# Optimization experiments

Measured on AMD Instinct MI355X. Metric: run time of the kernel, lower is better.

## Reference

```python
import jax, jax.numpy as jnp
import numpy as np

N_NODES = 51200
N_GRAPHS = 64
NODES_PER_GRAPH = 800
N_EDGES = 819200
DIM_IN = 128
DIM_HIDDEN = 64
HEADS = 3
DIM_OUT = 64


def leaky(x, slope):
    return jnp.where(x >= 0, x, slope * x)


def setup_inputs() -> dict:
    key = jax.random.key(0)
    ks = jax.random.split(key, 12)
    s = lambda fan_in: 1.0 / np.sqrt(fan_in)
    X = jax.random.normal(ks[0], (N_NODES, DIM_IN), dtype=jnp.float32)
    edge_indices = jax.random.randint(ks[1], (2, N_EDGES), 0, N_NODES, dtype=jnp.int32)
    ptr = (jnp.arange(N_GRAPHS + 1, dtype=jnp.int32) * NODES_PER_GRAPH)
    # linearSeq: Linear(dim_in, dim_hidden) + LeakyReLU
    W1 = jax.random.uniform(ks[2], (DIM_IN, DIM_HIDDEN), jnp.float32, -s(DIM_IN), s(DIM_IN))
    b1 = jax.random.uniform(ks[3], (DIM_HIDDEN,), jnp.float32, -s(DIM_IN), s(DIM_IN))
    # GATConv params: lin_src/lin_dst (no bias), att_src/att_dst, bias (concat=False -> out_channels)
    W_src = jax.random.uniform(ks[4], (DIM_HIDDEN, HEADS * DIM_HIDDEN), jnp.float32, -s(DIM_HIDDEN), s(DIM_HIDDEN))
    W_dst = jax.random.uniform(ks[5], (DIM_HIDDEN, HEADS * DIM_HIDDEN), jnp.float32, -s(DIM_HIDDEN), s(DIM_HIDDEN))
    att_src = jax.random.normal(ks[6], (HEADS, DIM_HIDDEN), dtype=jnp.float32) * 0.1
    att_dst = jax.random.normal(ks[7], (HEADS, DIM_HIDDEN), dtype=jnp.float32) * 0.1
    gat_bias = jnp.zeros((DIM_HIDDEN,), dtype=jnp.float32)
    # linear_final: Linear(2*dim_hidden, dim_out)
    Wf = jax.random.uniform(ks[8], (2 * DIM_HIDDEN, DIM_OUT), jnp.float32, -s(2 * DIM_HIDDEN), s(2 * DIM_HIDDEN))
    bf = jax.random.uniform(ks[9], (DIM_OUT,), jnp.float32, -s(2 * DIM_HIDDEN), s(2 * DIM_HIDDEN))
    return {"X": X, "W1": W1, "b1": b1, "W_src": W_src, "W_dst": W_dst,
            "att_src": att_src, "att_dst": att_dst, "gat_bias": gat_bias,
            "Wf": Wf, "bf": bf, "edge_indices": edge_indices, "ptr": ptr}


def reference(X, W1, b1, W_src, W_dst, att_src, att_dst, gat_bias, Wf, bf, edge_indices, ptr):
    N = X.shape[0]
    src, dst = edge_indices[0], edge_indices[1]  # message flows src -> dst
    # input projection
    h = leaky(X @ W1 + b1, 0.01)                                  # [N, DH]
    # GATConv (heads=3, concat=False, add_self_loops=False)
    x_src = (h @ W_src).reshape(N, HEADS, DIM_HIDDEN)             # [N, H, C]
    x_dst = (h @ W_dst).reshape(N, HEADS, DIM_HIDDEN)
    a_src = jnp.einsum('nhc,hc->nh', x_src, att_src)              # [N, H]
    a_dst = jnp.einsum('nhc,hc->nh', x_dst, att_dst)
    logits = leaky(a_src[src] + a_dst[dst], 0.2)                  # [E, H]
    # segment softmax over incoming edges of each target node
    m = jax.ops.segment_max(logits, dst, num_segments=N)          # [N, H]
    e = jnp.exp(logits - m[dst])
    denom = jax.ops.segment_sum(e, dst, num_segments=N)           # [N, H]
    attn = e / denom[dst]                                         # [E, H]
    msg = x_src[src] * attn[..., None]                            # [E, H, C]
    agg = jax.ops.segment_sum(msg, dst, num_segments=N)           # [N, H, C]
    out = agg.mean(axis=1) + gat_bias                             # concat=False -> head mean
    # final head
    cat = jnp.concatenate([h, out], axis=1)                       # [N, 2*DH]
    y = leaky(cat, 0.01) @ Wf + bf                                # [N, DO]
    # aggregate_using_ptr: mean-pool nodes per graph using CSR ptr
    node_graph = jnp.searchsorted(ptr, jnp.arange(N), side='right') - 1
    sums = jax.ops.segment_sum(y, node_graph, num_segments=ptr.shape[0] - 1)
    counts = (ptr[1:] - ptr[:-1]).astype(y.dtype)
    pooled = sums / counts[:, None]                               # [n_graphs, DO]
    return pooled, attn
```

## Files before the change

kernel.cpp:

```cpp
#include <hip/hip_runtime.h>
#include <hip/hip_bf16.h>

#define N_NODES   51200
#define N_GRAPHS  64
#define N_EDGES   819200
#define DIM_IN    128
#define DH        64
#define HEADS     3
#define DIM_OUT   64
#define CAP       96
#define NPART     8
#define PART_SZ   (N_NODES / NPART)
#define SC_BLOCKS (NPART * (N_EDGES / 2048))
#define K1_BLOCKS (N_NODES / 64)
#define P2_BLOCKS 80

typedef __hip_bfloat16 bf16;
typedef short bf16x8 __attribute__((ext_vector_type(8)));
typedef float f32x4  __attribute__((ext_vector_type(4)));

__device__ __forceinline__ float b2f(bf16 x) { return __bfloat162float(x); }
__device__ __forceinline__ bf16  f2b(float x) { return __float2bfloat16(x); }
__device__ __forceinline__ short f2bs(float x) { return (short)__bfloat16_as_ushort(f2b(x)); }
__device__ __forceinline__ float leaky(float x, float s) { return x >= 0.f ? x : s * x; }
__device__ __forceinline__ float ldin(const void* p, size_t i, int f32) {
    return f32 ? ((const float*)p)[i] : b2f(((const bf16*)p)[i]);
}
__device__ __forceinline__ bf16x8 ld8(const void* p, size_t i, int f32) {
    if (!f32) return *((const bf16x8*)((const short*)p + i));
    const float* f = (const float*)p + i;
    bf16x8 r;
    #pragma unroll
    for (int j = 0; j < 8; ++j) r[j] = f2bs(f[j]);
    return r;
}

__global__ __launch_bounds__(256) void detect_kernel(const unsigned short* __restrict__ Xu,
                                                     int* __restrict__ flag) {
    __shared__ int cnt;
    int tid = threadIdx.x;
    if (tid == 0) cnt = 0;
    __syncthreads();
    int local = 0;
    for (int i = tid * 2; i < 8192; i += 512) {
        unsigned e = (Xu[i] >> 7) & 0xFF;
        if (e >= 110 && e <= 135) local++;
    }
    atomicAdd(&cnt, local);
    __syncthreads();
    if (tid == 0) *flag = (cnt < 2048) ? 1 : 0;
}

__global__ __launch_bounds__(256) void prep1_kernel(const void* __restrict__ W1,
                                                    const void* __restrict__ Wsrc,
                                                    const void* __restrict__ Wdst,
                                                    const void* __restrict__ att_src,
                                                    const void* __restrict__ att_dst,
                                                    const int* __restrict__ flagp,
                                                    short* __restrict__ W1t,
                                                    short* __restrict__ Wat) {
    const int f32 = *flagp;
    int idx = blockIdx.x * 256 + threadIdx.x;
    if (idx < 8192) {
        int n = idx >> 7, k = idx & 127;
        W1t[idx] = f2bs(ldin(W1, (size_t)k * 64 + n, f32));
    } else if (idx < 9216) {
        int j = idx - 8192;
        int n = j >> 6, k = j & 63;
        float v = 0.f;
        if (n < 3) {
            for (int c = 0; c < 64; ++c)
                v += ldin(Wsrc, (size_t)k * 192 + n * 64 + c, f32) * ldin(att_src, n * 64 + c, f32);
        } else if (n < 6) {
            for (int c = 0; c < 64; ++c)
                v += ldin(Wdst, (size_t)k * 192 + (n - 3) * 64 + c, f32) * ldin(att_dst, (n - 3) * 64 + c, f32);
        }
        Wat[j] = f2bs(v);
    }
}

__global__ __launch_bounds__(256) void mega_kernel(const int* __restrict__ src,
                                                   const int* __restrict__ dst,
                                                   int* __restrict__ cursor,
                                                   unsigned short* __restrict__ bucket,
                                                   const void* __restrict__ X,
                                                   const short* __restrict__ W1t,
                                                   const short* __restrict__ Wat,
                                                   const void* __restrict__ b1,
                                                   const void* __restrict__ Wsrc,
                                                   const void* __restrict__ Wf,
                                                   const int* __restrict__ flagp,
                                                   bf16* __restrict__ h_bf,
                                                   unsigned char* __restrict__ h8,
                                                   float* __restrict__ a_src4,
                                                   float* __restrict__ a_dst4,
                                                   short* __restrict__ Wspt,
                                                   short* __restrict__ Wft) {
    if (blockIdx.x < SC_BLOCKS) {
        const int p = blockIdx.x & (NPART - 1);
        const int slice = blockIdx.x >> 3;
        const int lo = p * PART_SZ, hi = lo + PART_SZ;
        const int base = slice * 2048 + threadIdx.x;
        #pragma unroll
        for (int t = 0; t < 8; ++t) {
            int e = base + t * 256;
            int d = dst[e];
            if (d >= lo && d < hi) {
                int pos = atomicAdd(&cursor[d], 1);
                if (pos < CAP) bucket[(size_t)d * CAP + pos] = (unsigned short)src[e];
            }
        }
        return;
    }
    if (blockIdx.x >= SC_BLOCKS + K1_BLOCKS) {
        const int f32 = *flagp;
        int idx = (blockIdx.x - SC_BLOCKS - K1_BLOCKS) * 256 + threadIdx.x;
        if (idx < 12288) {
            int col = idx / 192;
            int rem = idx - col * 192;
            int hh = rem >> 6, kk = rem & 63;
            Wspt[idx] = f2bs(ldin(Wsrc, (size_t)kk * 192 + hh * 64 + col, f32) * (1.0f / 3.0f));
        } else {
            int j = idx - 12288;
            int n = j >> 7, k = j & 127;
            Wft[j] = f2bs(ldin(Wf, (size_t)k * 64 + n, f32));
        }
        return;
    }
    const int f32 = *flagp;
    __shared__ short hs[64 * 72];
    const int tid  = threadIdx.x;
    const int w    = tid >> 6;
    const int lane = tid & 63;
    const int lm   = lane & 15;
    const int q    = lane >> 4;
    const int row0 = (blockIdx.x - SC_BLOCKS) * 64;

    const float bias = ldin(b1, w * 16 + lm, f32);
    for (int mt = 0; mt < 4; ++mt) {
        f32x4 acc = {0.f, 0.f, 0.f, 0.f};
        #pragma unroll
        for (int kc = 0; kc < 4; ++kc) {
            bf16x8 a = ld8(X, (size_t)(row0 + mt * 16 + lm) * 128 + kc * 32 + q * 8, f32);
            bf16x8 b = *((const bf16x8*)(W1t + (size_t)(w * 16 + lm) * 128 + kc * 32 + q * 8));
            acc = __builtin_amdgcn_mfma_f32_16x16x32_bf16(a, b, acc, 0, 0, 0);
        }
        #pragma unroll
        for (int r = 0; r < 4; ++r) {
            int row = mt * 16 + q * 4 + r;
            float v = leaky(acc[r] + bias, 0.01f);
            short hv = f2bs(v);
            hs[row * 72 + w * 16 + lm] = hv;
            h_bf[(size_t)(row0 + row) * 64 + w * 16 + lm] = __ushort_as_bfloat16((unsigned short)hv);
            h8[(size_t)(row0 + row) * 64 + w * 16 + lm] =
                (unsigned char)__builtin_amdgcn_cvt_pk_fp8_f32(v, 0.f, 0, false);
        }
    }
    __syncthreads();

    {
        const int mt = w;
        bf16x8 a0  = *((const bf16x8*)(hs + (mt * 16 + lm) * 72 + q * 8));
        bf16x8 a1  = *((const bf16x8*)(hs + (mt * 16 + lm) * 72 + 32 + q * 8));
        bf16x8 b0  = *((const bf16x8*)(Wat + (size_t)lm * 64 + q * 8));
        bf16x8 b1v = *((const bf16x8*)(Wat + (size_t)lm * 64 + 32 + q * 8));
        f32x4 acca = {0.f, 0.f, 0.f, 0.f};
        acca = __builtin_amdgcn_mfma_f32_16x16x32_bf16(a0, b0, acca, 0, 0, 0);
        acca = __builtin_amdgcn_mfma_f32_16x16x32_bf16(a1, b1v, acca, 0, 0, 0);
        if (lm < 6) {
            #pragma unroll
            for (int r = 0; r < 4; ++r) {
                int row = row0 + mt * 16 + q * 4 + r;
                if (lm < 3) a_src4[(size_t)row * 4 + lm] = acca[r];
                else        a_dst4[(size_t)row * 4 + (lm - 3)] = acca[r];
            }
        }
    }
}

__global__ __launch_bounds__(256) void edge_kernel(const unsigned short* __restrict__ bucket,
                                                   const int* __restrict__ cursor,
                                                   const float* __restrict__ a_src4,
                                                   const float* __restrict__ a_dst4,
                                                   const unsigned char* __restrict__ h8,
                                                   float4* __restrict__ dstinfo,
                                                   bf16* __restrict__ wagg) {
    const int lane = threadIdx.x & 63;
    const int w = threadIdx.x >> 6;
    const int n = blockIdx.x * 4 + w;
    const int dg = min(cursor[n], CAP);
    const float4 ad = ((const float4*)a_dst4)[n];
    __shared__ float4 buf[4][64];
    float den0 = 0.f, den1 = 0.f, den2 = 0.f;
    float acc0 = 0.f, acc1 = 0.f, acc2 = 0.f;
    for (int c0 = 0; c0 < dg; c0 += 64) {
        int cnt = min(64, dg - c0);
        if (lane < cnt) {
            int s = bucket[n * CAP + c0 + lane];
            const float4 as = ((const float4*)a_src4)[s];
            float e0 = __expf(leaky(as.x + ad.x, 0.2f));
            float e1 = __expf(leaky(as.y + ad.y, 0.2f));
            float e2 = __expf(leaky(as.z + ad.z, 0.2f));
            den0 += e0; den1 += e1; den2 += e2;
            buf[w][lane] = make_float4(e0, e1, e2, __int_as_float(s));
        }
        asm volatile("s_waitcnt lgkmcnt(0)" ::: "memory");
        int j = 0;
        for (; j + 8 <= cnt; j += 8) {
            float4 r[8]; int hv[8];
            #pragma unroll
            for (int u = 0; u < 8; ++u) r[u] = buf[w][j + u];
            #pragma unroll
            for (int u = 0; u < 8; ++u)
                hv[u] = (int)h8[(((unsigned)__float_as_int(r[u].w)) << 6) | (unsigned)lane];
            #pragma unroll
            for (int u = 0; u < 8; ++u) {
                float f = __builtin_amdgcn_cvt_f32_fp8(hv[u], 0);
                acc0 += r[u].x * f; acc1 += r[u].y * f; acc2 += r[u].z * f;
            }
        }
        for (; j < cnt; ++j) {
            float4 r = buf[w][j];
            int hvv = (int)h8[(((unsigned)__float_as_int(r.w)) << 6) | (unsigned)lane];
            float f = __builtin_amdgcn_cvt_f32_fp8(hvv, 0);
            acc0 += r.x * f; acc1 += r.y * f; acc2 += r.z * f;
        }
    }
    #pragma unroll
    for (int off = 32; off >= 1; off >>= 1) {
        den0 += __shfl_xor(den0, off);
        den1 += __shfl_xor(den1, off);
        den2 += __shfl_xor(den2, off);
    }
    float inv0 = den0 > 0.f ? 1.f / den0 : 0.f;
    float inv1 = den1 > 0.f ? 1.f / den1 : 0.f;
    float inv2 = den2 > 0.f ? 1.f / den2 : 0.f;
    size_t wb = (size_t)n * 192;
    wagg[wb + lane]       = f2b(acc0 * inv0);
    wagg[wb + 64 + lane]  = f2b(acc1 * inv1);
    wagg[wb + 128 + lane] = f2b(acc2 * inv2);
    if (lane == 0) {
        dstinfo[(size_t)n * 2 + 0] = make_float4(ad.x, ad.y, ad.z, 0.f);
        dstinfo[(size_t)n * 2 + 1] = make_float4(inv0, inv1, inv2, 0.f);
    }
}

__global__ __launch_bounds__(256) void attn_g3_kernel(const int* __restrict__ src,
                                                      const int* __restrict__ dst,
                                                      const float* __restrict__ a_src4,
                                                      const float4* __restrict__ dstinfo,
                                                      const bf16* __restrict__ h_bf,
                                                      const bf16* __restrict__ wagg,
                                                      const short* __restrict__ Wspt,
                                                      const short* __restrict__ Wft,
                                                      const void* __restrict__ gat_bias,
                                                      const void* __restrict__ bfv,
                                                      const int* __restrict__ flagp,
                                                      bf16* __restrict__ y_bf,
                                                      void* __restrict__ d_out) {
    const int f32 = *flagp;
    __shared__ short cs[64 * 136];
    if (blockIdx.x < N_EDGES / 256) {
        int e = blockIdx.x * 256 + threadIdx.x;
        int s = src[e], d = dst[e];
        const float4 as = ((const float4*)a_src4)[s];
        const float4 ad = dstinfo[(size_t)d * 2 + 0];
        const float4 cv = dstinfo[(size_t)d * 2 + 1];
        float a0 = __expf(leaky(as.x + ad.x, 0.2f)) * cv.x;
        float a1 = __expf(leaky(as.y + ad.y, 0.2f)) * cv.y;
        float a2 = __expf(leaky(as.z + ad.z, 0.2f)) * cv.z;
        size_t o = (size_t)N_GRAPHS * DIM_OUT + (size_t)e * 3;
        if (f32) {
            float* p = (float*)d_out;
            p[o] = a0; p[o + 1] = a1; p[o + 2] = a2;
        } else {
            bf16* p = (bf16*)d_out;
            p[o] = f2b(a0); p[o + 1] = f2b(a1); p[o + 2] = f2b(a2);
        }
        return;
    }
    const int bid  = blockIdx.x - N_EDGES / 256;
    const int tid  = threadIdx.x;
    const int w    = tid >> 6;
    const int lane = tid & 63;
    const int lm   = lane & 15;
    const int q    = lane >> 4;
    const int row0 = bid * 64;
    for (int idx = tid; idx < 64 * 64; idx += 256) {
        int r = idx >> 6, k = idx & 63;
        cs[r * 136 + k] = f2bs(leaky(b2f(h_bf[(size_t)(row0 + r) * 64 + k]), 0.01f));
    }
    {
        const int col = w * 16 + lm;
        const float gb = ldin(gat_bias, col, f32);
        for (int mt = 0; mt < 4; ++mt) {
            f32x4 acc = {0.f, 0.f, 0.f, 0.f};
            #pragma unroll
            for (int kc = 0; kc < 6; ++kc) {
                bf16x8 a = *((const bf16x8*)((const short*)wagg + (size_t)(row0 + mt * 16 + lm) * 192 + kc * 32 + q * 8));
                bf16x8 b = *((const bf16x8*)(Wspt + (size_t)col * 192 + kc * 32 + q * 8));
                acc = __builtin_amdgcn_mfma_f32_16x16x32_bf16(a, b, acc, 0, 0, 0);
            }
            #pragma unroll
            for (int r = 0; r < 4; ++r) {
                int row = mt * 16 + q * 4 + r;
                cs[row * 136 + 64 + col] = f2bs(leaky(acc[r] + gb, 0.01f));
            }
        }
    }
    __syncthreads();
    const float bias = ldin(bfv, w * 16 + lm, f32);
    for (int mt = 0; mt < 4; ++mt) {
        f32x4 acc = {0.f, 0.f, 0.f, 0.f};
        #pragma unroll
        for (int kc = 0; kc < 4; ++kc) {
            bf16x8 a = *((const bf16x8*)(cs + (mt * 16 + lm) * 136 + kc * 32 + q * 8));
            bf16x8 b = *((const bf16x8*)(Wft + (size_t)(w * 16 + lm) * 128 + kc * 32 + q * 8));
            acc = __builtin_amdgcn_mfma_f32_16x16x32_bf16(a, b, acc, 0, 0, 0);
        }
        #pragma unroll
        for (int r = 0; r < 4; ++r) {
            int row = row0 + mt * 16 + q * 4 + r;
            y_bf[(size_t)row * 64 + w * 16 + lm] = f2b(acc[r] + bias);
        }
    }
}

__global__ __launch_bounds__(1024) void pool_kernel(const bf16* __restrict__ y_bf,
                                                    const int* __restrict__ ptr,
                                                    const int* __restrict__ flagp,
                                                    void* __restrict__ d_out) {
    __shared__ float part[16][64];
    const int f32 = *flagp;
    const int g = blockIdx.x;
    const int w = threadIdx.x >> 6, lane = threadIdx.x & 63;
    const int lo = ptr[g], hi = ptr[g + 1];
    const int cnt = hi - lo;
    float s = 0.f;
    for (int i = lo + w; i < hi; i += 16) s += b2f(y_bf[(size_t)i * DIM_OUT + lane]);
    part[w][lane] = s;
    __syncthreads();
    if (threadIdx.x < 64) {
        float t = 0.f;
        #pragma unroll
        for (int k = 0; k < 16; ++k) t += part[k][threadIdx.x];
        float v = t / (float)cnt;
        if (f32) ((float*)d_out)[g * DIM_OUT + threadIdx.x] = v;
        else     ((bf16*)d_out)[g * DIM_OUT + threadIdx.x]  = f2b(v);
    }
}

extern "C" void kernel_launch(void* const* d_in, const int* in_sizes, int n_in,
                              void* d_out, int out_size, void* d_ws, size_t ws_size,
                              hipStream_t stream) {
    const void* X        = d_in[0];
    const void* W1       = d_in[1];
    const void* b1       = d_in[2];
    const void* Wsrc     = d_in[3];
    const void* Wdst     = d_in[4];
    const void* att_src  = d_in[5];
    const void* att_dst  = d_in[6];
    const void* gat_bias = d_in[7];
    const void* Wf       = d_in[8];
    const void* bfv      = d_in[9];
    const int*  ei       = (const int*)d_in[10];
    const int*  ptr      = (const int*)d_in[11];
    const int*  src  = ei;
    const int*  dstp = ei + N_EDGES;

    char* ws = (char*)d_ws;
    size_t off_b = 0;
    auto alloc = [&](size_t bytes) -> char* {
        char* p = ws + off_b;
        off_b += (bytes + 255) & ~(size_t)255;
        return p;
    };
    int*     flag    = (int*)    alloc(256);
    short*   W1t     = (short*)  alloc(8192 * 2);
    short*   Wspt    = (short*)  alloc(12288 * 2);
    short*   Wft     = (short*)  alloc(8192 * 2);
    short*   Wat     = (short*)  alloc(1024 * 2);
    bf16*    h_bf    = (bf16*)   alloc((size_t)N_NODES * 64 * 2);
    unsigned char* h8 = (unsigned char*)alloc((size_t)N_NODES * 64);
    float*   a_src4  = (float*)  alloc((size_t)N_NODES * 16);
    float*   a_dst4  = (float*)  alloc((size_t)N_NODES * 16);
    float4*  dstinfo = (float4*) alloc((size_t)N_NODES * 2 * 16);
    bf16*    wagg    = (bf16*)   alloc((size_t)N_NODES * 192 * 2);
    int*     cursor  = (int*)    alloc((size_t)N_NODES * 4);
    unsigned short* bucket = (unsigned short*)alloc((size_t)N_NODES * CAP * 2);
    bf16*    y_bf    = (bf16*)   bucket;
    if (off_b > ws_size) return;

    hipLaunchKernelGGL(detect_kernel, dim3(1), dim3(256), 0, stream,
                       (const unsigned short*)X, flag);
    hipMemsetAsync(cursor, 0, (size_t)N_NODES * 4, stream);
    hipLaunchKernelGGL(prep1_kernel, dim3(36), dim3(256), 0, stream,
                       W1, Wsrc, Wdst, att_src, att_dst, flag, W1t, Wat);
    hipLaunchKernelGGL(mega_kernel, dim3(SC_BLOCKS + K1_BLOCKS + P2_BLOCKS), dim3(256), 0, stream,
                       src, dstp, cursor, bucket,
                       X, W1t, Wat, b1, Wsrc, Wf, flag,
                       h_bf, h8, a_src4, a_dst4, Wspt, Wft);
    hipLaunchKernelGGL(edge_kernel, dim3(N_NODES / 4), dim3(256), 0, stream,
                       bucket, cursor, a_src4, a_dst4, h8, dstinfo, wagg);
    hipLaunchKernelGGL(attn_g3_kernel, dim3(N_EDGES / 256 + N_NODES / 64), dim3(256), 0, stream,
                       src, dstp, a_src4, dstinfo, h_bf, wagg, Wspt, Wft,
                       gat_bias, bfv, flag, y_bf, d_out);
    hipLaunchKernelGGL(pool_kernel, dim3(N_GRAPHS), dim3(1024), 0, stream, y_bf, ptr, flag, d_out);
}
```

Measured before the change: 248.8 us.

## Pre-bin edges by destination partition before per-node bucket scatter

Adds a first pass that packs each edge's src and dst into one 32-bit word and appends it to one of eight partition buffers. It uses shared-memory counters and one global atomic per partition per block. The scatter pass then reads only its partition's compact list, so each edge is read once instead of eight times. Weight preprocessing is merged into the binning kernel and the prep kernel launch is removed. The cost is an extra kernel stage and buffer traffic, and the packing assumes node ids fit in 16 bits and each partition holds at most PBUF_CAP edges.

```diff
diff --git a/kernel.cpp b/kernel.cpp
--- a/kernel.cpp
+++ b/kernel.cpp
@@ -11,9 +11,11 @@
 #define CAP       96
 #define NPART     8
 #define PART_SZ   (N_NODES / NPART)
-#define SC_BLOCKS (NPART * (N_EDGES / 2048))
-#define K1_BLOCKS (N_NODES / 64)
-#define P2_BLOCKS 80
+#define PBUF_CAP  131072
+#define BIN_BLOCKS  (N_EDGES / 2048)
+#define PREP_BLOCKS 116
+#define SC2_BLOCKS  (NPART * (PBUF_CAP / 2048))
+#define K1_BLOCKS   (N_NODES / 64)
 
 typedef __hip_bfloat16 bf16;
 typedef short bf16x8 __attribute__((ext_vector_type(8)));
@@ -51,21 +53,66 @@
     if (tid == 0) *flag = (cnt < 2048) ? 1 : 0;
 }
 
-__global__ __launch_bounds__(256) void prep1_kernel(const void* __restrict__ W1,
-                                                    const void* __restrict__ Wsrc,
-                                                    const void* __restrict__ Wdst,
-                                                    const void* __restrict__ att_src,
-                                                    const void* __restrict__ att_dst,
-                                                    const int* __restrict__ flagp,
-                                                    short* __restrict__ W1t,
-                                                    short* __restrict__ Wat) {
+__global__ __launch_bounds__(256) void k_bin_prep(const int* __restrict__ src,
+                                                  const int* __restrict__ dst,
+                                                  int* __restrict__ pcur,
+                                                  unsigned* __restrict__ pbuf,
+                                                  const void* __restrict__ W1,
+                                                  const void* __restrict__ Wsrc,
+                                                  const void* __restrict__ Wdst,
+                                                  const void* __restrict__ Wf,
+                                                  const void* __restrict__ att_src,
+                                                  const void* __restrict__ att_dst,
+                                                  const int* __restrict__ flagp,
+                                                  short* __restrict__ W1t,
+                                                  short* __restrict__ Wspt,
+                                                  short* __restrict__ Wft,
+                                                  short* __restrict__ Wat) {
+    if (blockIdx.x < BIN_BLOCKS) {
+        __shared__ int cnt[NPART];
+        __shared__ int base[NPART];
+        const int tid = threadIdx.x;
+        if (tid < NPART) cnt[tid] = 0;
+        __syncthreads();
+        const int e0 = blockIdx.x * 2048;
+        unsigned pk[8]; int pp[8]; int rr[8];
+        #pragma unroll
+        for (int t = 0; t < 8; ++t) {
+            int e = e0 + t * 256 + tid;
+            int s = src[e], d = dst[e];
+            int p = d / PART_SZ;
+            pk[t] = ((unsigned)s << 16) | (unsigned)d;
+            pp[t] = p;
+            rr[t] = atomicAdd(&cnt[p], 1);
+        }
+        __syncthreads();
+        if (tid < NPART) base[tid] = atomicAdd(&pcur[tid], cnt[tid]);
+        __syncthreads();
+        #pragma unroll
+        for (int t = 0; t < 8; ++t) {
+            int p = pp[t];
+            int o = base[p] + rr[t];
+            if (o < PBUF_CAP) pbuf[(size_t)p * PBUF_CAP + o] = pk[t];
+        }
+        return;
+    }
     const int f32 = *flagp;
-    int idx = blockIdx.x * 256 + threadIdx.x;
+    int idx = (blockIdx.x - BIN_BLOCKS) * 256 + threadIdx.x;
     if (idx < 8192) {
         int n = idx >> 7, k = idx & 127;
         W1t[idx] = f2bs(ldin(W1, (size_t)k * 64 + n, f32));
-    } else if (idx < 9216) {
+    } else if (idx < 20480) {
         int j = idx - 8192;
+        int col = j / 192;
+        int rem = j - col * 192;
+        int hh = rem >> 6, kk = rem & 63;
+        Wspt[j] = f2bs(ldin(Wsrc, (size_t)kk * 192 + hh * 64 + col, f32) * (1.0f / 3.0f));
+    } else if (idx < 28672) {
+        int j = idx - 20480;
+        int n = j >> 7, k = j & 127;
+        Wft[j] = f2bs(ldin(Wf, (size_t)k * 64 + n, f32));
+    } else if (idx < 29696) {
+        int j = idx - 28672;
         int n = j >> 6, k = j & 63;
         float v = 0.f;
         if (n < 3) {
@@ -79,51 +126,34 @@
     }
 }
 
-__global__ __launch_bounds__(256) void mega_kernel(const int* __restrict__ src,
-                                                   const int* __restrict__ dst,
-                                                   int* __restrict__ cursor,
-                                                   unsigned short* __restrict__ bucket,
-                                                   const void* __restrict__ X,
-                                                   const short* __restrict__ W1t,
-                                                   const short* __restrict__ Wat,
-                                                   const void* __restrict__ b1,
-                                                   const void* __restrict__ Wsrc,
-                                                   const void* __restrict__ Wf,
-                                                   const int* __restrict__ flagp,
-                                                   bf16* __restrict__ h_bf,
-                                                   unsigned char* __restrict__ h8,
-                                                   float* __restrict__ a_src4,
-                                                   float* __restrict__ a_dst4,
-                                                   short* __restrict__ Wspt,
-                                                   short* __restrict__ Wft) {
-    if (blockIdx.x < SC_BLOCKS) {
+__global__ __launch_bounds__(256) void k_scatter_k1(const unsigned* __restrict__ pbuf,
+                                                    const int* __restrict__ pcur,
+                                                    int* __restrict__ cursor,
+                                                    unsigned short* __restrict__ bucket,
+                                                    const void* __restrict__ X,
+                                                    const short* __restrict__ W1t,
+                                                    const short* __restrict__ Wat,
+                                                    const void* __restrict__ b1,
+                                                    const int* __restrict__ flagp,
+                                                    bf16* __restrict__ h_bf,
+                                                    unsigned char* __restrict__ h8,
+                                                    float* __restrict__ a_src4,
+                                                    float* __restrict__ a_dst4) {
+    if (blockIdx.x < SC2_BLOCKS) {
         const int p = blockIdx.x & (NPART - 1);
         const int slice = blockIdx.x >> 3;
-        const int lo = p * PART_SZ, hi = lo + PART_SZ;
+        const int pc = min(pcur[p], PBUF_CAP);
+        const unsigned* pb = pbuf + (size_t)p * PBUF_CAP;
         const int base = slice * 2048 + threadIdx.x;
         #pragma unroll
         for (int t = 0; t < 8; ++t) {
-            int e = base + t * 256;
-            int d = dst[e];
-            if (d >= lo && d < hi) {
+            int i = base + t * 256;
+            if (i < pc) {
+                unsigned pk = pb[i];
+                int d = (int)(pk & 0xFFFFu);
                 int pos = atomicAdd(&cursor[d], 1);
-                if (pos < CAP) bucket[(size_t)d * CAP + pos] = (unsigned short)src[e];
+                if (pos < CAP) bucket[(size_t)d * CAP + pos] = (unsigned short)(pk >> 16);
             }
-        }
-        return;
-    }
-    if (blockIdx.x >= SC_BLOCKS + K1_BLOCKS) {
-        const int f32 = *flagp;
-        int idx = (blockIdx.x - SC_BLOCKS - K1_BLOCKS) * 256 + threadIdx.x;
-        if (idx < 12288) {
-            int col = idx / 192;
-            int rem = idx - col * 192;
-            int hh = rem >> 6, kk = rem & 63;
-            Wspt[idx] = f2bs(ldin(Wsrc, (size_t)kk * 192 + hh * 64 + col, f32) * (1.0f / 3.0f));
-        } else {
-            int j = idx - 12288;
-            int n = j >> 7, k = j & 127;
-            Wft[j] = f2bs(ldin(Wf, (size_t)k * 64 + n, f32));
         }
         return;
     }
@@ -134,7 +164,7 @@
     const int lane = tid & 63;
     const int lm   = lane & 15;
     const int q    = lane >> 4;
-    const int row0 = (blockIdx.x - SC_BLOCKS) * 64;
+    const int row0 = (blockIdx.x - SC2_BLOCKS) * 64;
 
     const float bias = ldin(b1, w * 16 + lm, f32);
     for (int mt = 0; mt < 4; ++mt) {
@@ -386,20 +416,22 @@
     float*   a_dst4  = (float*)  alloc((size_t)N_NODES * 16);
     float4*  dstinfo = (float4*) alloc((size_t)N_NODES * 2 * 16);
     bf16*    wagg    = (bf16*)   alloc((size_t)N_NODES * 192 * 2);
+    int*     pcur    = (int*)    alloc(256);
     int*     cursor  = (int*)    alloc((size_t)N_NODES * 4);
     unsigned short* bucket = (unsigned short*)alloc((size_t)N_NODES * CAP * 2);
+    unsigned* pbuf   = (unsigned*)wagg;
     bf16*    y_bf    = (bf16*)   bucket;
     if (off_b > ws_size) return;
 
     hipLaunchKernelGGL(detect_kernel, dim3(1), dim3(256), 0, stream,
                        (const unsigned short*)X, flag);
-    hipMemsetAsync(cursor, 0, (size_t)N_NODES * 4, stream);
-    hipLaunchKernelGGL(prep1_kernel, dim3(36), dim3(256), 0, stream,
-                       W1, Wsrc, Wdst, att_src, att_dst, flag, W1t, Wat);
-    hipLaunchKernelGGL(mega_kernel, dim3(SC_BLOCKS + K1_BLOCKS + P2_BLOCKS), dim3(256), 0, stream,
-                       src, dstp, cursor, bucket,
-                       X, W1t, Wat, b1, Wsrc, Wf, flag,
-                       h_bf, h8, a_src4, a_dst4, Wspt, Wft);
+    hipMemsetAsync(pcur, 0, 256 + (size_t)N_NODES * 4, stream);
+    hipLaunchKernelGGL(k_bin_prep, dim3(BIN_BLOCKS + PREP_BLOCKS), dim3(256), 0, stream,
+                       src, dstp, pcur, pbuf,
+                       W1, Wsrc, Wdst, Wf, att_src, att_dst, flag, W1t, Wspt, Wft, Wat);
+    hipLaunchKernelGGL(k_scatter_k1, dim3(SC2_BLOCKS + K1_BLOCKS), dim3(256), 0, stream,
+                       pbuf, pcur, cursor, bucket,
+                       X, W1t, Wat, b1, flag, h_bf, h8, a_src4, a_dst4);
     hipLaunchKernelGGL(edge_kernel, dim3(N_NODES / 4), dim3(256), 0, stream,
                        bucket, cursor, a_src4, a_dst4, h8, dstinfo, wagg);
     hipLaunchKernelGGL(attn_g3_kernel, dim3(N_EDGES / 256 + N_NODES / 64), dim3(256), 0, stream,
```

New measurement: 237.1 us. -4.7%, faster.
